# Kernel optimization log

Measured on AMD Instinct MI355X. Metric: run time of the kernel, lower is better.

Reference implementation:

```python
import jax, jax.numpy as jnp
import numpy as np

B, NI, NA, D = 16, 2048, 2048, 256

def setup_inputs() -> dict:
    key = jax.random.key(0)
    k1, k2, k3 = jax.random.split(key, 3)
    input_seq = jax.random.normal(k1, (B, NI, D), dtype=jnp.float32)
    attendee_seq = jax.random.normal(k2, (B, NA, D), dtype=jnp.float32)
    # glorot-ish scale for bilinear weight
    W = jax.random.normal(k3, (D, D), dtype=jnp.float32) * (1.0 / np.sqrt(D))
    return {"input_seq": input_seq, "attendee_seq": attendee_seq, "W": W}

def reference(input_seq, attendee_seq, W):
    # bilinear scores: (x_i W) . a_j   -> [B, NI, NA]
    xW = jnp.einsum('bid,de->bie', input_seq, W)
    scores = jnp.einsum('bie,bje->bij', xW, attendee_seq)
    A = jax.nn.softmax(scores, axis=2)                 # softmax over attendee axis
    # weighted context: sum_j A[b,i,j] * v[b,j,:] -> [B, NI, D]
    attended = jnp.einsum('bij,bjd->bid', A, attendee_seq)
    return attended
```

## Files before the change

kernel.cpp:

```cpp
#include <hip/hip_runtime.h>
#include <hip/hip_bf16.h>

#define BB 16
#define NI 2048
#define NA 2048
#define DD 256
#define KVB 32
#define NT (NA / KVB)

typedef _Float16 half8 __attribute__((ext_vector_type(8)));
typedef __attribute__((ext_vector_type(4))) float f32x4;
typedef __attribute__((ext_vector_type(4))) unsigned int uint4v;

typedef const unsigned int CGU __attribute__((address_space(1)));
typedef unsigned int LU __attribute__((address_space(3)));

static __device__ __forceinline__ unsigned short f2h(float f) {
  union { _Float16 h; unsigned short u; } x; x.h = (_Float16)f; return x.u;
}
static __device__ __forceinline__ float h2f(unsigned short u) {
  union { _Float16 h; unsigned short u; } x; x.u = u; return (float)x.h;
}
static __device__ __forceinline__ unsigned int pk2(float a, float b) {
  return __builtin_bit_cast(unsigned int, __builtin_amdgcn_cvt_pkrtz(a, b));
}
static __device__ __forceinline__ void gload16(const unsigned short* g, unsigned short* l) {
  __builtin_amdgcn_global_load_lds((CGU*)g, (LU*)l, 16, 0, 0);
}

__global__ void prep_kernel(const float* __restrict__ a,
                            unsigned short* __restrict__ kfrag,
                            unsigned short* __restrict__ vfrag,
                            const float* __restrict__ w,
                            unsigned short* __restrict__ wth,
                            unsigned short* __restrict__ wtl) {
  __shared__ float t[64][65];
  int bx = blockIdx.x;
  int tid = threadIdx.x;
  int rr = tid >> 4, c4 = tid & 15;

  if (bx >= 2048) {
    int r = bx - 2048;
    int dt = r >> 2, et = r & 3;
    int d0 = dt * 64, e0 = et * 64;
    int cc = c4 * 4;
#pragma unroll
    for (int k = 0; k < 4; ++k) {
      int row = rr + k * 16;
      float4 v = *(const float4*)(w + (size_t)(d0 + row) * DD + e0 + cc);
      t[row][cc + 0] = v.x; t[row][cc + 1] = v.y; t[row][cc + 2] = v.z; t[row][cc + 3] = v.w;
    }
    __syncthreads();
#pragma unroll
    for (int k = 0; k < 4; ++k) {
      int e = rr + k * 16;
      int eg = e0 + e;
      ushort4 h, l;
      float v0 = t[cc + 0][e]; h.x = f2h(v0); l.x = f2h(v0 - h2f(h.x));
      float v1 = t[cc + 1][e]; h.y = f2h(v1); l.y = f2h(v1 - h2f(h.y));
      float v2 = t[cc + 2][e]; h.z = f2h(v2); l.z = f2h(v2 - h2f(h.z));
      float v3 = t[cc + 3][e]; h.w = f2h(v3); l.w = f2h(v3 - h2f(h.w));
      int dd = d0 + cc;
      int u = dd >> 3, sub = dd & 7;
      size_t off = (size_t)eg * DD + ((u ^ (eg & 7)) * 8) + sub;
      *(ushort4*)(wth + off) = h;
      *(ushort4*)(wtl + off) = l;
    }
    return;
  }

  int b = bx >> 7;
  int r = bx & 127;
  int jt_t = r >> 2, dt_t = r & 3;
  int j0 = jt_t * 64, d0 = dt_t * 64;
#pragma unroll
  for (int k = 0; k < 4; ++k) {
    int row = rr + k * 16;
    int j = j0 + row;
    int d = d0 + c4 * 4;
    float4 v = *(const float4*)(a + ((size_t)b * NA + j) * DD + d);
    ushort4 hh;
    hh.x = f2h(v.x); hh.y = f2h(v.y); hh.z = f2h(v.z); hh.w = f2h(v.w);
    int kt = j >> 5, jtf = (j >> 4) & 1, l16k = j & 15;
    int c = d >> 5, quad = (d >> 3) & 3, e = d & 7;
    *(ushort4*)(kfrag + ((size_t)b * NT + kt) * 8192 + c * 1024 + jtf * 512 +
                (quad * 16 + l16k) * 8 + e) = hh;
    t[row][c4 * 4 + 0] = v.x; t[row][c4 * 4 + 1] = v.y;
    t[row][c4 * 4 + 2] = v.z; t[row][c4 * 4 + 3] = v.w;
  }
  __syncthreads();
#pragma unroll
  for (int k = 0; k < 4; ++k) {
    int dl = rr + k * 16;
    int d = d0 + dl;
    int j = j0 + c4 * 4;
    ushort4 o;
    o.x = f2h(t[c4 * 4 + 0][dl]); o.y = f2h(t[c4 * 4 + 1][dl]);
    o.z = f2h(t[c4 * 4 + 2][dl]); o.w = f2h(t[c4 * 4 + 3][dl]);
    int kt = j >> 5;
    int quad = c4 & 3;
    int jt = (c4 >> 2) & 1;
    int hh_ = (d >> 7) & 1, dtl = (d >> 4) & 7, l16v = d & 15;
    *(ushort4*)(vfrag + ((size_t)b * NT + kt) * 8192 + hh_ * 4096 + dtl * 512 +
                (quad * 16 + l16v) * 8 + jt * 4) = o;
  }
}

__global__ __launch_bounds__(256, 2) void qgemm_kernel(
    const float* __restrict__ x, const unsigned short* __restrict__ wth,
    const unsigned short* __restrict__ wtl, unsigned short* __restrict__ qf) {
  __shared__ unsigned short wb[2][64 * 256];
  const int tid = threadIdx.x;
  const int lane = tid & 63;
  const int wv = tid >> 6;
  const int quad = lane >> 4;
  const int l16 = lane & 15;
  const int m0 = blockIdx.x * 64;

  half8 xf[8];
  {
    const float* xr = x + (size_t)(m0 + wv * 16 + l16) * DD;
#pragma unroll
    for (int c = 0; c < 8; ++c) {
      float4 a = *(const float4*)(xr + c * 32 + quad * 8);
      float4 b = *(const float4*)(xr + c * 32 + quad * 8 + 4);
      half8 v;
      v[0] = (_Float16)a.x; v[1] = (_Float16)a.y; v[2] = (_Float16)a.z; v[3] = (_Float16)a.w;
      v[4] = (_Float16)b.x; v[5] = (_Float16)b.y; v[6] = (_Float16)b.z; v[7] = (_Float16)b.w;
      xf[c] = v;
    }
  }

#pragma unroll 1
  for (int eg = 0; eg < 4; ++eg) {
    uint4 t0[8], t1[8];
    {
      const unsigned short* sh = wth + (size_t)(eg * 64) * DD;
      const unsigned short* sl = wtl + (size_t)(eg * 64) * DD;
#pragma unroll
      for (int i = 0; i < 8; ++i) {
        t0[i] = *(const uint4*)(sh + (i * 256 + tid) * 8);
        t1[i] = *(const uint4*)(sl + (i * 256 + tid) * 8);
      }
    }
    __syncthreads();
#pragma unroll
    for (int i = 0; i < 8; ++i) {
      *(uint4*)(wb[0] + (i * 256 + tid) * 8) = t0[i];
      *(uint4*)(wb[1] + (i * 256 + tid) * 8) = t1[i];
    }
    __syncthreads();
#pragma unroll
    for (int etl = 0; etl < 4; ++etl) {
      int rloc = etl * 16 + l16;
      f32x4 acc; acc[0] = acc[1] = acc[2] = acc[3] = 0.f;
#pragma unroll
      for (int c = 0; c < 8; ++c) {
        int off = rloc * DD + (((4 * c + quad) ^ (rloc & 7)) * 8);
        half8 wh = *(const half8*)(wb[0] + off);
        half8 wl = *(const half8*)(wb[1] + off);
        acc = __builtin_amdgcn_mfma_f32_16x16x32_f16(xf[c], wh, acc, 0, 0, 0);
        acc = __builtin_amdgcn_mfma_f32_16x16x32_f16(xf[c], wl, acc, 0, 0, 0);
      }
      int e = eg * 64 + etl * 16 + l16;
#pragma unroll
      for (int rg = 0; rg < 4; ++rg) {
        qf[(size_t)(m0 + wv * 16 + 4 * quad + rg) * DD + e] = f2h(acc[rg] * 1.44269504f);
      }
    }
  }
}

__global__ __launch_bounds__(256, 4) void attn_kernel(
    const unsigned short* __restrict__ kfrag, const unsigned short* __restrict__ vfrag,
    const unsigned short* __restrict__ qf, float* __restrict__ out) {
  __shared__ unsigned short kls[2][KVB * DD];

  const int tid = threadIdx.x;
  const int lane = tid & 63;
  const int wv = tid >> 6;
  const int p = wv >> 1;
  const int h = wv & 1;
  const int quad = lane >> 4;
  const int l16 = lane & 15;

  int bx = blockIdx.x;
  int lbx = (bx & 7) * 128 + (bx >> 3);
  const int b = lbx >> 6;
  const int qbase = (lbx & 63) * 32 + p * 16;

  const unsigned short* kfb = kfrag + (size_t)b * NT * 8192;
  const unsigned short* vfb = vfrag + (size_t)b * NT * 8192 + h * 4096;

  half8 qh[8];
  {
    const size_t qrow = ((size_t)b * NI + qbase + l16) * DD;
#pragma unroll
    for (int c = 0; c < 8; ++c)
      qh[c] = *(const half8*)(qf + qrow + c * 32 + quad * 8);
  }

  f32x4 acc[8];
#pragma unroll
  for (int dt = 0; dt < 8; ++dt) { acc[dt][0] = 0.f; acc[dt][1] = 0.f; acc[dt][2] = 0.f; acc[dt][3] = 0.f; }
  float m0r = -INFINITY;
  float l0 = 0.f;

#pragma unroll
  for (int i = 0; i < 4; ++i) {
    int off = (i * 4 + wv) * 512;
    gload16(kfb + off + lane * 8, &kls[0][off]);
  }
  __syncthreads();

#pragma unroll 1
  for (int kt = 0; kt < NT; ++kt) {
    half8 vb[8];
#pragma unroll
    for (int dt = 0; dt < 8; ++dt)
      vb[dt] = *(const half8*)(vfb + (size_t)kt * 8192 + dt * 512 + lane * 8);

    if (kt + 1 < NT) {
      const unsigned short* s = kfb + (size_t)(kt + 1) * 8192;
      unsigned short* d = &kls[(kt + 1) & 1][0];
#pragma unroll
      for (int i = 0; i < 4; ++i) {
        int off = (i * 4 + wv) * 512;
        gload16(s + off + lane * 8, d + off);
      }
    }

    const unsigned short* kb = &kls[kt & 1][0];
    f32x4 sa0, sb0, sa1, sb1;
    sa0[0]=sa0[1]=sa0[2]=sa0[3]=0.f; sb0[0]=sb0[1]=sb0[2]=sb0[3]=0.f;
    sa1[0]=sa1[1]=sa1[2]=sa1[3]=0.f; sb1[0]=sb1[1]=sb1[2]=sb1[3]=0.f;
    __builtin_amdgcn_s_setprio(1);
#pragma unroll
    for (int c = 0; c < 4; ++c) {
      half8 k0 = *(const half8*)(kb + c * 1024 + lane * 8);
      half8 k1 = *(const half8*)(kb + c * 1024 + 512 + lane * 8);
      sa0 = __builtin_amdgcn_mfma_f32_16x16x32_f16(k0, qh[c], sa0, 0, 0, 0);
      sa1 = __builtin_amdgcn_mfma_f32_16x16x32_f16(k1, qh[c], sa1, 0, 0, 0);
    }
#pragma unroll
    for (int c = 4; c < 8; ++c) {
      half8 k0 = *(const half8*)(kb + c * 1024 + lane * 8);
      half8 k1 = *(const half8*)(kb + c * 1024 + 512 + lane * 8);
      sb0 = __builtin_amdgcn_mfma_f32_16x16x32_f16(k0, qh[c], sb0, 0, 0, 0);
      sb1 = __builtin_amdgcn_mfma_f32_16x16x32_f16(k1, qh[c], sb1, 0, 0, 0);
    }
    __builtin_amdgcn_s_setprio(0);
    f32x4 st0, st1;
    st0[0]=sa0[0]+sb0[0]; st0[1]=sa0[1]+sb0[1]; st0[2]=sa0[2]+sb0[2]; st0[3]=sa0[3]+sb0[3];
    st1[0]=sa1[0]+sb1[0]; st1[1]=sa1[1]+sb1[1]; st1[2]=sa1[2]+sb1[2]; st1[3]=sa1[3]+sb1[3];

    float mt = fmaxf(fmaxf(fmaxf(st0[0], st0[1]), fmaxf(st0[2], st0[3])),
                     fmaxf(fmaxf(st1[0], st1[1]), fmaxf(st1[2], st1[3])));
    if (__any(mt > m0r + 11.5416f)) {
      float mr = fmaxf(mt, __shfl_xor(mt, 16));
      mr = fmaxf(mr, __shfl_xor(mr, 32));
      float mn = fmaxf(m0r, mr);
      float sc = exp2f(m0r - mn);
      l0 *= sc;
#pragma unroll
      for (int rg = 0; rg < 4; ++rg) {
        float a0 = __shfl(sc, 4 * quad + rg);
#pragma unroll
        for (int dt = 0; dt < 8; ++dt) acc[dt][rg] *= a0;
      }
      m0r = mn;
    }

    float e00 = exp2f(st0[0] - m0r), e01 = exp2f(st0[1] - m0r);
    float e02 = exp2f(st0[2] - m0r), e03 = exp2f(st0[3] - m0r);
    float e10 = exp2f(st1[0] - m0r), e11 = exp2f(st1[1] - m0r);
    float e12 = exp2f(st1[2] - m0r), e13 = exp2f(st1[3] - m0r);
    l0 += ((e00 + e01) + (e02 + e03)) + ((e10 + e11) + (e12 + e13));
    half8 pa;
    {
      uint4v pau = { pk2(e00, e01), pk2(e02, e03), pk2(e10, e11), pk2(e12, e13) };
      pa = __builtin_bit_cast(half8, pau);
    }

    __builtin_amdgcn_s_setprio(1);
#pragma unroll
    for (int dt = 0; dt < 8; ++dt)
      acc[dt] = __builtin_amdgcn_mfma_f32_16x16x32_f16(pa, vb[dt], acc[dt], 0, 0, 0);
    __builtin_amdgcn_s_setprio(0);

    __syncthreads();
  }

  l0 += __shfl_xor(l0, 16); l0 += __shfl_xor(l0, 32);
  float inv0 = 1.0f / l0;
  size_t ob = ((size_t)b * NI + qbase) * DD + h * 128;
#pragma unroll
  for (int rg = 0; rg < 4; ++rg) {
    float i0 = __shfl(inv0, 4 * quad + rg);
#pragma unroll
    for (int dt = 0; dt < 8; ++dt) {
      int d = dt * 16 + l16;
      out[ob + (size_t)(4 * quad + rg) * DD + d] = acc[dt][rg] * i0;
    }
  }
}

extern "C" void kernel_launch(void* const* d_in, const int* in_sizes, int n_in,
                              void* d_out, int out_size, void* d_ws, size_t ws_size,
                              hipStream_t stream) {
  const float* x = (const float*)d_in[0];
  const float* att = (const float*)d_in[1];
  const float* W = (const float*)d_in[2];
  float* out = (float*)d_out;

  const size_t NE = (size_t)BB * NA * DD;
  unsigned short* w0    = (unsigned short*)d_ws;
  unsigned short* kfrag = w0;
  unsigned short* vfrag = w0 + NE;
  unsigned short* qfp   = w0 + 2 * NE;
  unsigned short* wth   = w0 + 3 * NE;
  unsigned short* wtl   = w0 + 3 * NE + (size_t)DD * DD;

  prep_kernel<<<2064, 256, 0, stream>>>(att, kfrag, vfrag, W, wth, wtl);
  qgemm_kernel<<<512, 256, 0, stream>>>(x, wth, wtl, qfp);
  attn_kernel<<<1024, 256, 0, stream>>>(kfrag, vfrag, qfp, out);
}
```

Before: 201.5 us.

## Split QK^T across wave pair and exchange score halves via LDS

Before this change, the two waves sharing a query tile (h=0/1) each computed the full 32-key score block, duplicating the QK^T MFMAs. Now each wave computes only its 16-key half and swaps the half-precision scores with its partner through a small double-buffered LDS array. The loop's barrier moves to sit between the score exchange and the softmax. This halves score MFMA work per wave but rounds the partner's scores to fp16 before exp, and it places a barrier in the middle of the dependent chain, which may cost latency.

```diff
diff --git a/kernel.cpp b/kernel.cpp
--- a/kernel.cpp
+++ b/kernel.cpp
@@ -9,6 +9,7 @@
 #define NT (NA / KVB)
 
 typedef _Float16 half8 __attribute__((ext_vector_type(8)));
+typedef _Float16 half2t __attribute__((ext_vector_type(2)));
 typedef __attribute__((ext_vector_type(4))) float f32x4;
 typedef __attribute__((ext_vector_type(4))) unsigned int uint4v;
 
@@ -175,6 +176,7 @@
     const unsigned short* __restrict__ kfrag, const unsigned short* __restrict__ vfrag,
     const unsigned short* __restrict__ qf, float* __restrict__ out) {
   __shared__ unsigned short kls[2][KVB * DD];
+  __shared__ uint2 sx[2][2][2][64];
 
   const int tid = threadIdx.x;
   const int lane = tid & 63;
@@ -231,31 +233,35 @@
     }
 
     const unsigned short* kb = &kls[kt & 1][0];
-    f32x4 sa0, sb0, sa1, sb1;
-    sa0[0]=sa0[1]=sa0[2]=sa0[3]=0.f; sb0[0]=sb0[1]=sb0[2]=sb0[3]=0.f;
-    sa1[0]=sa1[1]=sa1[2]=sa1[3]=0.f; sb1[0]=sb1[1]=sb1[2]=sb1[3]=0.f;
+    f32x4 sa, sb;
+    sa[0]=sa[1]=sa[2]=sa[3]=0.f; sb[0]=sb[1]=sb[2]=sb[3]=0.f;
     __builtin_amdgcn_s_setprio(1);
 #pragma unroll
     for (int c = 0; c < 4; ++c) {
-      half8 k0 = *(const half8*)(kb + c * 1024 + lane * 8);
-      half8 k1 = *(const half8*)(kb + c * 1024 + 512 + lane * 8);
-      sa0 = __builtin_amdgcn_mfma_f32_16x16x32_f16(k0, qh[c], sa0, 0, 0, 0);
-      sa1 = __builtin_amdgcn_mfma_f32_16x16x32_f16(k1, qh[c], sa1, 0, 0, 0);
+      half8 k0 = *(const half8*)(kb + c * 1024 + h * 512 + lane * 8);
+      sa = __builtin_amdgcn_mfma_f32_16x16x32_f16(k0, qh[c], sa, 0, 0, 0);
     }
 #pragma unroll
     for (int c = 4; c < 8; ++c) {
-      half8 k0 = *(const half8*)(kb + c * 1024 + lane * 8);
-      half8 k1 = *(const half8*)(kb + c * 1024 + 512 + lane * 8);
-      sb0 = __builtin_amdgcn_mfma_f32_16x16x32_f16(k0, qh[c], sb0, 0, 0, 0);
-      sb1 = __builtin_amdgcn_mfma_f32_16x16x32_f16(k1, qh[c], sb1, 0, 0, 0);
+      half8 k0 = *(const half8*)(kb + c * 1024 + h * 512 + lane * 8);
+      sb = __builtin_amdgcn_mfma_f32_16x16x32_f16(k0, qh[c], sb, 0, 0, 0);
     }
     __builtin_amdgcn_s_setprio(0);
-    f32x4 st0, st1;
-    st0[0]=sa0[0]+sb0[0]; st0[1]=sa0[1]+sb0[1]; st0[2]=sa0[2]+sb0[2]; st0[3]=sa0[3]+sb0[3];
-    st1[0]=sa1[0]+sb1[0]; st1[1]=sa1[1]+sb1[1]; st1[2]=sa1[2]+sb1[2]; st1[3]=sa1[3]+sb1[3];
-
-    float mt = fmaxf(fmaxf(fmaxf(st0[0], st0[1]), fmaxf(st0[2], st0[3])),
-                     fmaxf(fmaxf(st1[0], st1[1]), fmaxf(st1[2], st1[3])));
+    f32x4 s;
+    s[0] = sa[0] + sb[0]; s[1] = sa[1] + sb[1];
+    s[2] = sa[2] + sb[2]; s[3] = sa[3] + sb[3];
+
+    sx[kt & 1][p][h][lane] = make_uint2(pk2(s[0], s[1]), pk2(s[2], s[3]));
+    __syncthreads();
+
+    uint2 ox = sx[kt & 1][p][h ^ 1][lane];
+    half2t oa = __builtin_bit_cast(half2t, ox.x);
+    half2t ob = __builtin_bit_cast(half2t, ox.y);
+    float o0 = (float)oa[0], o1 = (float)oa[1];
+    float o2 = (float)ob[0], o3 = (float)ob[1];
+
+    float mt = fmaxf(fmaxf(fmaxf(s[0], s[1]), fmaxf(s[2], s[3])),
+                     fmaxf(fmaxf(o0, o1), fmaxf(o2, o3)));
     if (__any(mt > m0r + 11.5416f)) {
       float mr = fmaxf(mt, __shfl_xor(mt, 16));
       mr = fmaxf(mr, __shfl_xor(mr, 32));
@@ -271,24 +277,23 @@
       m0r = mn;
     }
 
-    float e00 = exp2f(st0[0] - m0r), e01 = exp2f(st0[1] - m0r);
-    float e02 = exp2f(st0[2] - m0r), e03 = exp2f(st0[3] - m0r);
-    float e10 = exp2f(st1[0] - m0r), e11 = exp2f(st1[1] - m0r);
-    float e12 = exp2f(st1[2] - m0r), e13 = exp2f(st1[3] - m0r);
-    l0 += ((e00 + e01) + (e02 + e03)) + ((e10 + e11) + (e12 + e13));
-    half8 pa;
-    {
-      uint4v pau = { pk2(e00, e01), pk2(e02, e03), pk2(e10, e11), pk2(e12, e13) };
-      pa = __builtin_bit_cast(half8, pau);
-    }
+    float es0 = exp2f(s[0] - m0r), es1 = exp2f(s[1] - m0r);
+    float es2 = exp2f(s[2] - m0r), es3 = exp2f(s[3] - m0r);
+    float eo0 = exp2f(o0 - m0r), eo1 = exp2f(o1 - m0r);
+    float eo2 = exp2f(o2 - m0r), eo3 = exp2f(o3 - m0r);
+    l0 += ((es0 + es1) + (es2 + es3)) + ((eo0 + eo1) + (eo2 + eo3));
+    unsigned int d0 = pk2(es0, es1), d1 = pk2(es2, es3);
+    unsigned int c0 = pk2(eo0, eo1), c1 = pk2(eo2, eo3);
+    uint4v pau;
+    if (h == 0) { pau[0] = d0; pau[1] = d1; pau[2] = c0; pau[3] = c1; }
+    else        { pau[0] = c0; pau[1] = c1; pau[2] = d0; pau[3] = d1; }
+    half8 pa = __builtin_bit_cast(half8, pau);
 
     __builtin_amdgcn_s_setprio(1);
 #pragma unroll
     for (int dt = 0; dt < 8; ++dt)
       acc[dt] = __builtin_amdgcn_mfma_f32_16x16x32_f16(pa, vb[dt], acc[dt], 0, 0, 0);
     __builtin_amdgcn_s_setprio(0);
-
-    __syncthreads();
   }
 
   l0 += __shfl_xor(l0, 16); l0 += __shfl_xor(l0, 32);
```

After: 196.5 us. 2.4% less time.
